# Performance work log

Hardware: AMD Instinct MI355X
Metric: run time of the kernel (lower is better)

## Reference

```python
import jax, jax.numpy as jnp
import numpy as np

B, C, H, W = 2, 256, 96, 96
KC = 32  # key_channels


def setup_inputs() -> dict:
    key = jax.random.key(0)
    ks = jax.random.split(key, 10)
    s_in = 1.0 / np.sqrt(C)
    s_kc = 1.0 / np.sqrt(KC)
    return {
        "x": jax.random.normal(ks[0], (B, C, H, W), jnp.float32),
        "human": jax.random.normal(ks[1], (B, C, H, W), jnp.float32),
        "Wq": jax.random.normal(ks[2], (KC, C), jnp.float32) * s_in,
        "bq": jnp.zeros((KC,), jnp.float32),
        "Wd": jax.random.normal(ks[3], (KC, C), jnp.float32) * s_in,
        "bd": jnp.zeros((KC,), jnp.float32),
        "Wf": jax.random.normal(ks[4], (KC, KC), jnp.float32) * s_kc,
        "bf": jnp.zeros((KC,), jnp.float32),
        "Wu": jax.random.normal(ks[5], (C, KC), jnp.float32) * s_kc,
        "bu": jnp.zeros((C,), jnp.float32),
    }


def reference(x, human, Wq, bq, Wd, bd, Wf, bf, Wu, bu):
    b, c, h, w = x.shape
    kc = Wq.shape[0]
    n = h * w
    # 1x1 conv projections == per-pixel matmul
    q = (jnp.einsum('bchw,kc->bkhw', human, Wq) + bq[None, :, None, None]).reshape(b, kc, n)
    # sim_map = scale * q^T q over spatial positions, softmax over last dim
    sim = jnp.einsum('bkn,bkm->bnm', q, q) * (kc ** -0.5)  # (b, n, n)
    sim = jax.nn.softmax(sim, axis=-1)
    v = (jnp.einsum('bchw,kc->bkhw', x, Wd) + bd[None, :, None, None]).reshape(b, kc, n)
    # context[b, n, k] = sim @ v^T  -> back to (b, kc, h, w)
    ctx = jnp.einsum('bnm,bkm->bkn', sim, v).reshape(b, kc, h, w)
    # f: 1x1 conv + bias + ReLU (ConvModule default act)
    ctx = jax.nn.relu(jnp.einsum('bkhw,jk->bjhw', ctx, Wf) + bf[None, :, None, None])
    # f_up: 1x1 conv + bias, no activation (act_cfg=None)
    ctx = jnp.einsum('bkhw,ck->bchw', ctx, Wu) + bu[None, :, None, None]
    return x + ctx
```

## Files before the change

### kernel.cpp

```cpp
#include <hip/hip_runtime.h>
#include <hip/hip_bf16.h>

#define NB 2
#define CCH 256
#define NPIX 9216
#define KCH 32
#define NTILE 288
#define SQSCALE 0.5050098f

#define QPA_B 73728u
#define VBS_B 294912u

typedef __attribute__((ext_vector_type(8)))  short short8;
typedef __attribute__((ext_vector_type(16))) float f32x16;
typedef __attribute__((ext_vector_type(4)))  unsigned uint4v;

union ABu { unsigned u[4]; uint4v v4; short8 s; };

__device__ __forceinline__ unsigned pk2(float a, float b) {
  __hip_bfloat162 h = __float22bfloat162_rn(make_float2(a, b));
  unsigned r; __builtin_memcpy(&r, &h, 4); return r;
}
__device__ __forceinline__ unsigned short bf1(float a) {
  __hip_bfloat16 h = __float2bfloat16(a);
  unsigned short r; __builtin_memcpy(&r, &h, 2); return r;
}
__device__ __forceinline__ float bfx(unsigned short h) {
  unsigned v = ((unsigned)h) << 16;
  float f; __builtin_memcpy(&f, &v, 4); return f;
}
__device__ __forceinline__ void split_pk(float a, float b, unsigned &hp, unsigned &lp) {
  unsigned short ha = bf1(a), hb_ = bf1(b);
  hp = (unsigned)ha | ((unsigned)hb_ << 16);
  unsigned short la = bf1(a - bfx(ha)), lb = bf1(b - bfx(hb_));
  lp = (unsigned)la | ((unsigned)lb << 16);
}
__device__ __forceinline__ void plswap(unsigned &a, unsigned &b) {
  auto r = __builtin_amdgcn_permlane32_swap(a, b, false, false);
  a = r[0]; b = r[1];
}

#define MFMA32(a, b, c) __builtin_amdgcn_mfma_f32_32x32x16_bf16((a), (b), (c), 0, 0, 0)

__global__ __launch_bounds__(256) void proj_mfma(
    const float* __restrict__ x, const float* __restrict__ human,
    const float* __restrict__ Wq, const float* __restrict__ bq,
    const float* __restrict__ Wd, const float* __restrict__ bd,
    unsigned* __restrict__ qPA,
    unsigned* __restrict__ qPB,
    unsigned short* __restrict__ vBS)
{
  __shared__ float4 slab[4][8][64];
  const int tid = threadIdx.x;
  const int w   = tid >> 6;
  const int l   = tid & 63;
  const int hi  = l >> 5;
  const int ql  = l & 31;
  const int blk = blockIdx.x;
  const int b   = blk / NTILE;
  const int tN  = blk % NTILE;
  const int n0  = tN * 32;
  const int c0  = w * 64;
  const float* hb = human + (size_t)b*CCH*NPIX;
  const float* xb = x + (size_t)b*CCH*NPIX;

  ABu aqh[4], aqlo[4], adh[4], adlo[4];
#pragma unroll
  for (int s = 0; s < 4; ++s) {
    const int cbase = c0 + 16*s + 8*hi;
#pragma unroll
    for (int j = 0; j < 4; ++j) {
      const float q0 = Wq[ql*CCH + cbase + 2*j], q1 = Wq[ql*CCH + cbase + 2*j + 1];
      const float d0 = Wd[ql*CCH + cbase + 2*j], d1 = Wd[ql*CCH + cbase + 2*j + 1];
      split_pk(q0, q1, aqh[s].u[j], aqlo[s].u[j]);
      split_pk(d0, d1, adh[s].u[j], adlo[s].u[j]);
    }
  }

  f32x16 qa, va;
#pragma unroll
  for (int r = 0; r < 16; ++r) { qa[r] = 0.f; va[r] = 0.f; }

#pragma unroll
  for (int s = 0; s < 4; ++s) {
    const int cbase = c0 + 16*s + 8*hi;
    ABu bhh, bhl, bxh, bxl;
#pragma unroll
    for (int j = 0; j < 4; ++j) {
      const float h0 = hb[(size_t)(cbase + 2*j  )*NPIX + n0 + ql];
      const float h1 = hb[(size_t)(cbase + 2*j+1)*NPIX + n0 + ql];
      const float x0 = xb[(size_t)(cbase + 2*j  )*NPIX + n0 + ql];
      const float x1 = xb[(size_t)(cbase + 2*j+1)*NPIX + n0 + ql];
      split_pk(h0, h1, bhh.u[j], bhl.u[j]);
      split_pk(x0, x1, bxh.u[j], bxl.u[j]);
    }
    qa = MFMA32(aqh[s].s,  bhh.s, qa);
    qa = MFMA32(aqh[s].s,  bhl.s, qa);
    qa = MFMA32(aqlo[s].s, bhh.s, qa);
    va = MFMA32(adh[s].s,  bxh.s, va);
    va = MFMA32(adh[s].s,  bxl.s, va);
    va = MFMA32(adlo[s].s, bxh.s, va);
  }

#pragma unroll
  for (int jf = 0; jf < 4; ++jf) {
    slab[w][jf  ][l] = make_float4(qa[4*jf], qa[4*jf+1], qa[4*jf+2], qa[4*jf+3]);
    slab[w][4+jf][l] = make_float4(va[4*jf], va[4*jf+1], va[4*jf+2], va[4*jf+3]);
  }
  __syncthreads();
  if (w == 0) {
    unsigned* qpa = qPA + (size_t)b*QPA_B;
    unsigned* qpb = qPB + (size_t)b*QPA_B;
    unsigned short* vbs = vBS + (size_t)b*VBS_B;
#pragma unroll
    for (int jf = 0; jf < 4; ++jf) {
      const int kc = 8*jf + 4*hi;
      float4 s0 = slab[0][jf][l], s1 = slab[1][jf][l], s2 = slab[2][jf][l], s3 = slab[3][jf][l];
      const float v0 = (s0.x+s1.x+s2.x+s3.x + bq[kc+0]) * SQSCALE;
      const float v1 = (s0.y+s1.y+s2.y+s3.y + bq[kc+1]) * SQSCALE;
      const float v2 = (s0.z+s1.z+s2.z+s3.z + bq[kc+2]) * SQSCALE;
      const float v3 = (s0.w+s1.w+s2.w+s3.w + bq[kc+3]) * SQSCALE;
      const int p0 = 4*jf + 2*hi;
      unsigned* a0p = (p0 < 8) ? qpa : qpb;
      a0p[(size_t)tN*256 + ((p0&7)>>2)*128 + ql*4 + (p0&3)] = pk2(v0, v1);
      const int p1 = p0 + 1;
      unsigned* a1p = (p1 < 8) ? qpa : qpb;
      a1p[(size_t)tN*256 + ((p1&7)>>2)*128 + ql*4 + (p1&3)] = pk2(v2, v3);
      float4 t0 = slab[0][4+jf][l], t1 = slab[1][4+jf][l], t2 = slab[2][4+jf][l], t3 = slab[3][4+jf][l];
      const size_t vbase = (size_t)tN*1024 + (size_t)(ql>>4)*512 + (size_t)(ql&15);
      vbs[vbase + (size_t)(kc+0)*16] = bf1(t0.x+t1.x+t2.x+t3.x + bd[kc+0]);
      vbs[vbase + (size_t)(kc+1)*16] = bf1(t0.y+t1.y+t2.y+t3.y + bd[kc+1]);
      vbs[vbase + (size_t)(kc+2)*16] = bf1(t0.z+t1.z+t2.z+t3.z + bd[kc+2]);
      vbs[vbase + (size_t)(kc+3)*16] = bf1(t0.w+t1.w+t2.w+t3.w + bd[kc+3]);
    }
  }
}

__global__ __launch_bounds__(512, 6) void attn_mfma(
    const unsigned* __restrict__ qPA, const unsigned* __restrict__ qPB,
    const unsigned short* __restrict__ vBS,
    float* __restrict__ ctx)
{
  __shared__ float slab[8][32][32];
  __shared__ float mlbuf[8][32];
  const int tid = threadIdx.x;
  const int w   = tid >> 6;
  const int l   = tid & 63;
  const int hi  = l >> 5;
  const int ql  = l & 31;
  const int blk = blockIdx.x;
  const int b   = blk / NTILE;
  const int tq  = blk % NTILE;
  const int q0  = tq * 32;

  const unsigned* qa_ = qPA + (size_t)b*QPA_B;
  const unsigned* qb_ = qPB + (size_t)b*QPA_B;
  const unsigned short* vb_ = vBS + (size_t)b*VBS_B;

  ABu bq1, bq2;
  bq1.v4 = *(const uint4v*)(qa_ + (size_t)tq*256 + hi*128 + ql*4);
  bq2.v4 = *(const uint4v*)(qb_ + (size_t)tq*256 + hi*128 + ql*4);

  f32x16 O;
#pragma unroll
  for (int r = 0; r < 16; ++r) O[r] = 0.f;
  float lsum = 0.f;

  for (int it = 0; it < 36; ++it) {
    const int t = it*8 + w;
    const size_t ko = (size_t)t*256 + hi*128 + ql*4;
    ABu ak1, ak2;
    ak1.v4 = *(const uint4v*)(qa_ + ko);
    ak2.v4 = *(const uint4v*)(qb_ + ko);
    const size_t vo = (size_t)t*1024 + (size_t)ql*16 + hi*8;
    const short8 av1 = *(const short8*)(vb_ + vo);
    const short8 av2 = *(const short8*)(vb_ + vo + 512);

    f32x16 s;
#pragma unroll
    for (int r = 0; r < 16; ++r) s[r] = 0.f;
    s = MFMA32(ak1.s, bq1.s, s);
    s = MFMA32(ak2.s, bq2.s, s);

    float p[16];
#pragma unroll
    for (int r = 0; r < 16; ++r) p[r] = __builtin_amdgcn_exp2f(s[r]);
    lsum += (((p[0]+p[1])+(p[2]+p[3])) + ((p[4]+p[5])+(p[6]+p[7])))
          + (((p[8]+p[9])+(p[10]+p[11])) + ((p[12]+p[13])+(p[14]+p[15])));

    unsigned a0 = pk2(p[0],  p[1]),  a1 = pk2(p[2],  p[3]);
    unsigned b0 = pk2(p[4],  p[5]),  b1 = pk2(p[6],  p[7]);
    unsigned a2 = pk2(p[8],  p[9]),  a3 = pk2(p[10], p[11]);
    unsigned b2 = pk2(p[12], p[13]), b3 = pk2(p[14], p[15]);
    plswap(a0, b0); plswap(a1, b1); plswap(a2, b2); plswap(a3, b3);
    ABu pb1, pb2;
    pb1.u[0] = a0; pb1.u[1] = a1; pb1.u[2] = b0; pb1.u[3] = b1;
    pb2.u[0] = a2; pb2.u[1] = a3; pb2.u[2] = b2; pb2.u[3] = b3;

    O = MFMA32(av1, pb1.s, O);
    O = MFMA32(av2, pb2.s, O);
  }

  lsum += __shfl_xor(lsum, 32);
  if (hi == 0) mlbuf[w][ql] = lsum;
#pragma unroll
  for (int r = 0; r < 16; ++r)
    slab[w][(r&3) + 8*(r>>2) + 4*hi][ql] = O[r];
  __syncthreads();

  {
    const int q  = tid & 31;
    const int kh = tid >> 5;
    float L = 0.f;
#pragma unroll
    for (int ww = 0; ww < 8; ++ww) L += mlbuf[ww][q];
    const float inv = 1.f / L;
#pragma unroll
    for (int i = 0; i < 2; ++i) {
      const int kc = kh + 16*i;
      float acc = 0.f;
#pragma unroll
      for (int ww = 0; ww < 8; ++ww) acc += slab[ww][kc][q];
      ctx[((size_t)b*KCH + kc)*NPIX + q0 + q] = acc * inv;
    }
  }
}

__global__ __launch_bounds__(64) void epi_kernel(
    const float* __restrict__ x, const float* __restrict__ ctx,
    const float* __restrict__ Wf, const float* __restrict__ bf,
    const float* __restrict__ Wu, const float* __restrict__ bu,
    float* __restrict__ out)
{
  __shared__ float4 swf[256];
  __shared__ float4 swu[512];
  const int lane = threadIdx.x;
  const int blk = blockIdx.x;
  const int pb = blk % 288;
  const int cq = blk / 288;
  const int b = pb / 144;
  const int n = (pb % 144)*64 + lane;
#pragma unroll
  for (int it = 0; it < 4; ++it) swf[it*64 + lane] = ((const float4*)Wf)[it*64 + lane];
#pragma unroll
  for (int it = 0; it < 8; ++it) swu[it*64 + lane] = ((const float4*)Wu)[cq*512 + it*64 + lane];
  __syncthreads();
  const float* cb = ctx + b*KCH*NPIX + n;
  float cv[KCH];
#pragma unroll
  for (int k = 0; k < KCH; ++k) cv[k] = cb[k*NPIX];
  float gv[KCH];
#pragma unroll
  for (int j = 0; j < KCH; ++j) {
    float acc = bf[j];
#pragma unroll
    for (int w = 0; w < 8; ++w) {
      const float4 wv = swf[j*8 + w];
      acc += wv.x*cv[4*w+0] + wv.y*cv[4*w+1] + wv.z*cv[4*w+2] + wv.w*cv[4*w+3];
    }
    gv[j] = fmaxf(acc, 0.f);
  }
  const float* xb = x + (b*CCH + cq*64)*NPIX + n;
  float* ob = out + (b*CCH + cq*64)*NPIX + n;
#pragma unroll 4
  for (int c = 0; c < 64; ++c) {
    float acc = bu[cq*64 + c];
#pragma unroll
    for (int w = 0; w < 8; ++w) {
      const float4 wv = swu[c*8 + w];
      acc += wv.x*gv[4*w+0] + wv.y*gv[4*w+1] + wv.z*gv[4*w+2] + wv.w*gv[4*w+3];
    }
    ob[c*NPIX] = xb[c*NPIX] + acc;
  }
}

extern "C" void kernel_launch(void* const* d_in, const int* in_sizes, int n_in,
                              void* d_out, int out_size, void* d_ws, size_t ws_size,
                              hipStream_t stream) {
  (void)in_sizes; (void)n_in; (void)out_size; (void)ws_size;
  const float* x     = (const float*)d_in[0];
  const float* human = (const float*)d_in[1];
  const float* Wq    = (const float*)d_in[2];
  const float* bq    = (const float*)d_in[3];
  const float* Wd    = (const float*)d_in[4];
  const float* bd    = (const float*)d_in[5];
  const float* Wf    = (const float*)d_in[6];
  const float* bf    = (const float*)d_in[7];
  const float* Wu    = (const float*)d_in[8];
  const float* bu    = (const float*)d_in[9];
  float* out = (float*)d_out;

  unsigned* qPA       = (unsigned*)d_ws;
  unsigned* qPB       = qPA + (size_t)NB*QPA_B;
  unsigned short* vBS = (unsigned short*)(qPB + (size_t)NB*QPA_B);
  float* ctx          = (float*)(vBS + (size_t)NB*VBS_B);

  proj_mfma<<<576, 256, 0, stream>>>(x, human, Wq, bq, Wd, bd, qPA, qPB, vBS);
  attn_mfma<<<576, 512, 0, stream>>>(qPA, qPB, vBS, ctx);
  epi_kernel<<<1152, 64, 0, stream>>>(x, ctx, Wf, bf, Wu, bu, out);
}
```

Measured before the change: 182.0 us.

## Split attention into single-wave split-K partials with separate merge kernel

Replaces the 512-thread attention block with single-wave blocks. Each block handles two query tiles over a 1/16 key slice, so every key/value load feeds two MFMA chains, and the blocks are swizzled across the grid. Partial outputs and row sums go to workspace and a new merge kernel reduces them into ctx. The epilogue is also split into 32-channel chunks to double its grid. This trades extra workspace traffic and a third launch for more parallelism and reuse of the K/V fragments. The old attention path is kept as a fallback when the workspace is too small.

Measured after the change: 181.5 us. About the same (-0.2%).

```diff
diff --git a/kernel.cpp b/kernel.cpp
--- a/kernel.cpp
+++ b/kernel.cpp
@@ -136,6 +136,132 @@
   }
 }
 
+__global__ __launch_bounds__(64, 4) void attn_wave(
+    const unsigned* __restrict__ qPA, const unsigned* __restrict__ qPB,
+    const unsigned short* __restrict__ vBS,
+    float4* __restrict__ pO4,
+    float* __restrict__ pL)
+{
+  const int l   = threadIdx.x;
+  const int hi  = l >> 5;
+  const int ql  = l & 31;
+  const int blk = blockIdx.x;
+  const int swz = (blk & 7)*576 + (blk >> 3);
+  const int b   = swz / 2304;
+  const int r2  = swz % 2304;
+  const int qt  = r2 >> 4;
+  const int ks  = r2 & 15;
+
+  const unsigned* qa_ = qPA + (size_t)b*QPA_B;
+  const unsigned* qb_ = qPB + (size_t)b*QPA_B;
+  const unsigned short* vb_ = vBS + (size_t)b*VBS_B;
+
+  ABu bqA1, bqA2, bqB1, bqB2;
+  bqA1.v4 = *(const uint4v*)(qa_ + (size_t)(2*qt  )*256 + hi*128 + ql*4);
+  bqA2.v4 = *(const uint4v*)(qb_ + (size_t)(2*qt  )*256 + hi*128 + ql*4);
+  bqB1.v4 = *(const uint4v*)(qa_ + (size_t)(2*qt+1)*256 + hi*128 + ql*4);
+  bqB2.v4 = *(const uint4v*)(qb_ + (size_t)(2*qt+1)*256 + hi*128 + ql*4);
+
+  f32x16 OA, OB, Z;
+#pragma unroll
+  for (int r = 0; r < 16; ++r) { OA[r] = 0.f; OB[r] = 0.f; Z[r] = 0.f; }
+  float lsA = 0.f, lsB = 0.f;
+
+  for (int it = 0; it < 18; ++it) {
+    const int t = ks*18 + it;
+    const size_t ko = (size_t)t*256 + hi*128 + ql*4;
+    ABu ak1, ak2;
+    ak1.v4 = *(const uint4v*)(qa_ + ko);
+    ak2.v4 = *(const uint4v*)(qb_ + ko);
+    const size_t vo = (size_t)t*1024 + (size_t)ql*16 + hi*8;
+    const short8 av1 = *(const short8*)(vb_ + vo);
+    const short8 av2 = *(const short8*)(vb_ + vo + 512);
+
+    f32x16 s = MFMA32(ak1.s, bqA1.s, Z);
+    s = MFMA32(ak2.s, bqA2.s, s);
+    float p[16];
+#pragma unroll
+    for (int r = 0; r < 16; ++r) p[r] = __builtin_amdgcn_exp2f(s[r]);
+    lsA += (((p[0]+p[1])+(p[2]+p[3])) + ((p[4]+p[5])+(p[6]+p[7])))
+         + (((p[8]+p[9])+(p[10]+p[11])) + ((p[12]+p[13])+(p[14]+p[15])));
+    {
+      unsigned a0 = pk2(p[0],p[1]),  a1 = pk2(p[2],p[3]);
+      unsigned b0 = pk2(p[4],p[5]),  b1 = pk2(p[6],p[7]);
+      unsigned a2 = pk2(p[8],p[9]),  a3 = pk2(p[10],p[11]);
+      unsigned b2 = pk2(p[12],p[13]),b3 = pk2(p[14],p[15]);
+      plswap(a0,b0); plswap(a1,b1); plswap(a2,b2); plswap(a3,b3);
+      ABu pb1, pb2;
+      pb1.u[0]=a0; pb1.u[1]=a1; pb1.u[2]=b0; pb1.u[3]=b1;
+      pb2.u[0]=a2; pb2.u[1]=a3; pb2.u[2]=b2; pb2.u[3]=b3;
+      OA = MFMA32(av1, pb1.s, OA);
+      OA = MFMA32(av2, pb2.s, OA);
+    }
+    s = MFMA32(ak1.s, bqB1.s, Z);
+    s = MFMA32(ak2.s, bqB2.s, s);
+#pragma unroll
+    for (int r = 0; r < 16; ++r) p[r] = __builtin_amdgcn_exp2f(s[r]);
+    lsB += (((p[0]+p[1])+(p[2]+p[3])) + ((p[4]+p[5])+(p[6]+p[7])))
+         + (((p[8]+p[9])+(p[10]+p[11])) + ((p[12]+p[13])+(p[14]+p[15])));
+    {
+      unsigned a0 = pk2(p[0],p[1]),  a1 = pk2(p[2],p[3]);
+      unsigned b0 = pk2(p[4],p[5]),  b1 = pk2(p[6],p[7]);
+      unsigned a2 = pk2(p[8],p[9]),  a3 = pk2(p[10],p[11]);
+      unsigned b2 = pk2(p[12],p[13]),b3 = pk2(p[14],p[15]);
+      plswap(a0,b0); plswap(a1,b1); plswap(a2,b2); plswap(a3,b3);
+      ABu pb1, pb2;
+      pb1.u[0]=a0; pb1.u[1]=a1; pb1.u[2]=b0; pb1.u[3]=b1;
+      pb2.u[0]=a2; pb2.u[1]=a3; pb2.u[2]=b2; pb2.u[3]=b3;
+      OB = MFMA32(av1, pb1.s, OB);
+      OB = MFMA32(av2, pb2.s, OB);
+    }
+  }
+
+  lsA += __shfl_xor(lsA, 32);
+  lsB += __shfl_xor(lsB, 32);
+#pragma unroll
+  for (int rq = 0; rq < 4; ++rq) {
+    pO4[((size_t)swz*8 + rq    )*64 + l] = make_float4(OA[4*rq], OA[4*rq+1], OA[4*rq+2], OA[4*rq+3]);
+    pO4[((size_t)swz*8 + 4 + rq)*64 + l] = make_float4(OB[4*rq], OB[4*rq+1], OB[4*rq+2], OB[4*rq+3]);
+  }
+  if (l < 32) {
+    pL[(size_t)swz*64 + l]      = lsA;
+    pL[(size_t)swz*64 + 32 + l] = lsB;
+  }
+}
+
+__global__ __launch_bounds__(64) void attn_merge(
+    const float4* __restrict__ pO4, const float* __restrict__ pL,
+    float* __restrict__ ctx)
+{
+  const int l   = threadIdx.x;
+  const int blk = blockIdx.x;
+  const int b   = blk / 576;
+  const int rem = blk % 576;
+  const int qt  = rem >> 2;
+  const int kcq = rem & 3;
+  const int f   = l >> 5;
+  const int qlm = l & 31;
+
+  float ax=0,ay=0,az=0,aw=0, bx=0,by=0,bz=0,bw=0, L=0;
+  const size_t base = (size_t)b*2304 + (size_t)qt*16;
+#pragma unroll 4
+  for (int ks = 0; ks < 16; ++ks) {
+    const size_t pb_ = base + ks;
+    const float4* pp = pO4 + (pb_*8 + (size_t)f*4 + kcq)*64;
+    const float4 t0 = pp[qlm];
+    const float4 t1 = pp[qlm + 32];
+    ax += t0.x; ay += t0.y; az += t0.z; aw += t0.w;
+    bx += t1.x; by += t1.y; bz += t1.z; bw += t1.w;
+    L  += pL[pb_*64 + l];
+  }
+  const float inv = 1.f / L;
+  float* cb = ctx + ((size_t)b*KCH + kcq*8)*NPIX + (size_t)qt*64 + l;
+  cb[0*NPIX] = ax*inv;  cb[1*NPIX] = ay*inv;
+  cb[2*NPIX] = az*inv;  cb[3*NPIX] = aw*inv;
+  cb[4*NPIX] = bx*inv;  cb[5*NPIX] = by*inv;
+  cb[6*NPIX] = bz*inv;  cb[7*NPIX] = bw*inv;
+}
+
 __global__ __launch_bounds__(512, 6) void attn_mfma(
     const unsigned* __restrict__ qPA, const unsigned* __restrict__ qPB,
     const unsigned short* __restrict__ vBS,
@@ -188,14 +314,14 @@
     lsum += (((p[0]+p[1])+(p[2]+p[3])) + ((p[4]+p[5])+(p[6]+p[7])))
           + (((p[8]+p[9])+(p[10]+p[11])) + ((p[12]+p[13])+(p[14]+p[15])));
 
-    unsigned a0 = pk2(p[0],  p[1]),  a1 = pk2(p[2],  p[3]);
-    unsigned b0 = pk2(p[4],  p[5]),  b1 = pk2(p[6],  p[7]);
-    unsigned a2 = pk2(p[8],  p[9]),  a3 = pk2(p[10], p[11]);
-    unsigned b2 = pk2(p[12], p[13]), b3 = pk2(p[14], p[15]);
-    plswap(a0, b0); plswap(a1, b1); plswap(a2, b2); plswap(a3, b3);
+    unsigned a0 = pk2(p[0],p[1]),  a1 = pk2(p[2],p[3]);
+    unsigned b0 = pk2(p[4],p[5]),  b1 = pk2(p[6],p[7]);
+    unsigned a2 = pk2(p[8],p[9]),  a3 = pk2(p[10],p[11]);
+    unsigned b2 = pk2(p[12],p[13]),b3 = pk2(p[14],p[15]);
+    plswap(a0,b0); plswap(a1,b1); plswap(a2,b2); plswap(a3,b3);
     ABu pb1, pb2;
-    pb1.u[0] = a0; pb1.u[1] = a1; pb1.u[2] = b0; pb1.u[3] = b1;
-    pb2.u[0] = a2; pb2.u[1] = a3; pb2.u[2] = b2; pb2.u[3] = b3;
+    pb1.u[0]=a0; pb1.u[1]=a1; pb1.u[2]=b0; pb1.u[3]=b1;
+    pb2.u[0]=a2; pb2.u[1]=a3; pb2.u[2]=b2; pb2.u[3]=b3;
 
     O = MFMA32(av1, pb1.s, O);
     O = MFMA32(av2, pb2.s, O);
@@ -226,29 +352,29 @@
   }
 }
 
-__global__ __launch_bounds__(64) void epi_kernel(
+__global__ __launch_bounds__(64) void epi_kernel8(
     const float* __restrict__ x, const float* __restrict__ ctx,
     const float* __restrict__ Wf, const float* __restrict__ bf,
     const float* __restrict__ Wu, const float* __restrict__ bu,
     float* __restrict__ out)
 {
   __shared__ float4 swf[256];
-  __shared__ float4 swu[512];
+  __shared__ float4 swu[256];
   const int lane = threadIdx.x;
   const int blk = blockIdx.x;
   const int pb = blk % 288;
-  const int cq = blk / 288;
+  const int co = blk / 288;
   const int b = pb / 144;
   const int n = (pb % 144)*64 + lane;
 #pragma unroll
   for (int it = 0; it < 4; ++it) swf[it*64 + lane] = ((const float4*)Wf)[it*64 + lane];
 #pragma unroll
-  for (int it = 0; it < 8; ++it) swu[it*64 + lane] = ((const float4*)Wu)[cq*512 + it*64 + lane];
+  for (int it = 0; it < 4; ++it) swu[it*64 + lane] = ((const float4*)Wu)[co*256 + it*64 + lane];
   __syncthreads();
-  const float* cb = ctx + b*KCH*NPIX + n;
+  const float* cb = ctx + (size_t)b*KCH*NPIX + n;
   float cv[KCH];
 #pragma unroll
-  for (int k = 0; k < KCH; ++k) cv[k] = cb[k*NPIX];
+  for (int k = 0; k < KCH; ++k) cv[k] = cb[(size_t)k*NPIX];
   float gv[KCH];
 #pragma unroll
   for (int j = 0; j < KCH; ++j) {
@@ -260,24 +386,24 @@
     }
     gv[j] = fmaxf(acc, 0.f);
   }
-  const float* xb = x + (b*CCH + cq*64)*NPIX + n;
-  float* ob = out + (b*CCH + cq*64)*NPIX + n;
+  const float* xb = x + ((size_t)b*CCH + co*32)*NPIX + n;
+  float* ob = out + ((size_t)b*CCH + co*32)*NPIX + n;
 #pragma unroll 4
-  for (int c = 0; c < 64; ++c) {
-    float acc = bu[cq*64 + c];
+  for (int c = 0; c < 32; ++c) {
+    float acc = bu[co*32 + c];
 #pragma unroll
     for (int w = 0; w < 8; ++w) {
       const float4 wv = swu[c*8 + w];
       acc += wv.x*gv[4*w+0] + wv.y*gv[4*w+1] + wv.z*gv[4*w+2] + wv.w*gv[4*w+3];
     }
-    ob[c*NPIX] = xb[c*NPIX] + acc;
+    ob[(size_t)c*NPIX] = xb[(size_t)c*NPIX] + acc;
   }
 }
 
 extern "C" void kernel_launch(void* const* d_in, const int* in_sizes, int n_in,
                               void* d_out, int out_size, void* d_ws, size_t ws_size,
                               hipStream_t stream) {
-  (void)in_sizes; (void)n_in; (void)out_size; (void)ws_size;
+  (void)in_sizes; (void)n_in; (void)out_size;
   const float* x     = (const float*)d_in[0];
   const float* human = (const float*)d_in[1];
   const float* Wq    = (const float*)d_in[2];
@@ -294,8 +420,17 @@
   unsigned* qPB       = qPA + (size_t)NB*QPA_B;
   unsigned short* vBS = (unsigned short*)(qPB + (size_t)NB*QPA_B);
   float* ctx          = (float*)(vBS + (size_t)NB*VBS_B);
+  float4* pO4         = (float4*)(ctx + (size_t)NB*KCH*NPIX);
+  float* pL           = (float*)(pO4 + (size_t)4608*8*64);
+
+  const size_t need = ((char*)(pL + (size_t)4608*64)) - (char*)d_ws;
 
   proj_mfma<<<576, 256, 0, stream>>>(x, human, Wq, bq, Wd, bd, qPA, qPB, vBS);
-  attn_mfma<<<576, 512, 0, stream>>>(qPA, qPB, vBS, ctx);
-  epi_kernel<<<1152, 64, 0, stream>>>(x, ctx, Wf, bf, Wu, bu, out);
-}
+  if (ws_size >= need) {
+    attn_wave<<<4608, 64, 0, stream>>>(qPA, qPB, vBS, pO4, pL);
+    attn_merge<<<1152, 64, 0, stream>>>(pO4, pL, ctx);
+  } else {
+    attn_mfma<<<576, 512, 0, stream>>>(qPA, qPB, vBS, ctx);
+  }
+  epi_kernel8<<<2304, 64, 0, stream>>>(x, ctx, Wf, bf, Wu, bu, out);
+}
```
